# Kernel optimization log

Measured on AMD Instinct MI355X. Metric: run time of the kernel, lower is better.

Reference implementation:

```python
import jax, jax.numpy as jnp
import numpy as np


def setup_inputs() -> dict:
    key = jax.random.key(0)
    k1, k2, k3, k4 = jax.random.split(key, 4)
    B, S, I, O, G = 4, 2048, 4096, 11008, 128
    x = jax.random.normal(k1, (B, S, I), dtype=jnp.float32)
    # unpacked int4 codes in [0, 16)
    weight_q = jax.random.randint(k2, (O, I), 0, 16, dtype=jnp.int32)
    scales = jax.random.uniform(k3, (I // G, O, 1), minval=0.001, maxval=0.02)
    zeros = jax.random.normal(k4, (I // G, O, 1)) * 0.01
    scales_and_zeros = jnp.concatenate([scales, zeros], axis=-1).astype(jnp.bfloat16)
    return {"x": x, "weight_q": weight_q, "scales_and_zeros": scales_and_zeros, "groupsize": G}


def reference(x, weight_q, scales_and_zeros, groupsize):
    # Dequantize: w[o, g*gs + j] = (q - 8) * scale[g, o] + zero[g, o], in bf16
    O, I = weight_q.shape
    G = I // groupsize
    q = weight_q.reshape(O, G, groupsize).astype(jnp.bfloat16)  # [O, G, gs]
    s = scales_and_zeros[:, :, 0].T[:, :, None]  # [O, G, 1]
    z = scales_and_zeros[:, :, 1].T[:, :, None]  # [O, G, 1]
    w = ((q - 8.0) * s + z).reshape(O, I)  # bf16 dequantized weight
    xb = x.astype(jnp.bfloat16).reshape(-1, I)
    y = jnp.matmul(xb, w.T)  # [N, O] in bf16 (matches precision=bf16)
    y = y.astype(x.dtype)
    return y.reshape(x.shape[:-1] + (O,))
```

## Files before the change

### kernel.cpp

```cpp
#include <hip/hip_runtime.h>
#include <cstdint>
#include <cstddef>

#define N_ 8192
#define K_ 4096
#define O_ 11008
#define NT_ (K_ / 32)

typedef __bf16 bf16x8 __attribute__((ext_vector_type(8)));
typedef float f32x4 __attribute__((ext_vector_type(4)));

__device__ __forceinline__ uint16_t f2bf(float f) {
    uint32_t u = __float_as_uint(f);
    u += 0x7fffu + ((u >> 16) & 1u);
    return (uint16_t)(u >> 16);
}
__device__ __forceinline__ float bf2f(uint16_t b) {
    return __uint_as_float(((uint32_t)b) << 16);
}
__device__ __forceinline__ float bfr(float f) { return bf2f(f2bf(f)); }

__device__ __forceinline__ void async_cp16(const uint16_t* gsrc, uint16_t* ldst) {
    __builtin_amdgcn_global_load_lds(
        (__attribute__((address_space(1))) void*)gsrc,
        (__attribute__((address_space(3))) void*)ldst, 16, 0, 0);
}

__global__ __launch_bounds__(256) void xcast(const float* __restrict__ X,
                                             uint16_t* __restrict__ Xb) {
    const size_t n8 = (size_t)N_ * K_ / 8;
    size_t i = (size_t)blockIdx.x * 256u + threadIdx.x;
    const size_t stride = (size_t)gridDim.x * 256u;
    for (; i < n8; i += stride) {
        float4 a = ((const float4*)X)[2 * i];
        float4 b = ((const float4*)X)[2 * i + 1];
        union { uint16_t u[8]; uint4 v; } r;
        r.u[0] = f2bf(a.x); r.u[1] = f2bf(a.y); r.u[2] = f2bf(a.z); r.u[3] = f2bf(a.w);
        r.u[4] = f2bf(b.x); r.u[5] = f2bf(b.y); r.u[6] = f2bf(b.z); r.u[7] = f2bf(b.w);
        ((uint4*)Xb)[i] = r.v;
    }
}

__global__ __launch_bounds__(256) void wdeq(const int* __restrict__ Q,
                                            const float* __restrict__ SZ,
                                            uint16_t* __restrict__ Wb) {
    const size_t n8 = (size_t)O_ * K_ / 8;
    size_t i = (size_t)blockIdx.x * 256u + threadIdx.x;
    const size_t stride = (size_t)gridDim.x * 256u;
    for (; i < n8; i += stride) {
        const size_t e = i * 8;
        const size_t o = e >> 12;
        const uint32_t g = ((uint32_t)e >> 7) & 31;
        const float2 sz = ((const float2*)SZ)[(size_t)g * O_ + o];
        const float s = bfr(sz.x);
        const float z = bfr(sz.y);
        int4 qa = ((const int4*)Q)[2 * i];
        int4 qb = ((const int4*)Q)[2 * i + 1];
        int qs[8] = {qa.x, qa.y, qa.z, qa.w, qb.x, qb.y, qb.z, qb.w};
        union { uint16_t u[8]; uint4 v; } r;
#pragma unroll
        for (int j = 0; j < 8; ++j) {
            r.u[j] = f2bf(bfr((float)(qs[j] - 8) * s) + z);
        }
        ((uint4*)Wb)[i] = r.v;
    }
}

__global__ __launch_bounds__(512, 2) void gemm_mfma1b(const uint16_t* __restrict__ A,
                                                      const uint16_t* __restrict__ B,
                                                      float* __restrict__ C) {
    __shared__ uint16_t sA[4][256 * 32];
    __shared__ uint16_t sB[4][256 * 32];

    const int tid = threadIdx.x;
    const int l = tid & 63;
    const int w = tid >> 6;
    const int wm = w >> 2;
    const int wn = w & 3;
    const int n0 = blockIdx.x * 256;
    const int o0 = blockIdx.y * 256;

    const int gk = (((tid & 3) ^ ((tid >> 3) & 3)) & 3) * 8;
    const int sr0 = tid >> 2;
    const uint16_t* gA0 = A + (size_t)(n0 + sr0) * K_ + gk;
    const uint16_t* gA1 = A + (size_t)(n0 + 128 + sr0) * K_ + gk;
    const uint16_t* gB0 = B + (size_t)(o0 + sr0) * K_ + gk;
    const uint16_t* gB1 = B + (size_t)(o0 + 128 + sr0) * K_ + gk;
    const int ldst = tid * 8;

    const int lr = l & 15;
    const int cph = (((l >> 4) ^ ((l >> 1) & 3)) & 3) * 8;

    f32x4 acc[8][4] = {};

#define STAGE_A(j)                                                      \
    {                                                                   \
        const size_t ko = (size_t)(j) * 32;                             \
        uint16_t* d = &sA[(j) & 3][ldst];                               \
        async_cp16(gA0 + ko, d);                                        \
        async_cp16(gA1 + ko, d + 4096);                                 \
    }
#define STAGE_B(j)                                                      \
    {                                                                   \
        const size_t ko = (size_t)(j) * 32;                             \
        uint16_t* d = &sB[(j) & 3][ldst];                               \
        async_cp16(gB0 + ko, d);                                        \
        async_cp16(gB1 + ko, d + 4096);                                 \
    }

    STAGE_A(0) STAGE_B(0)
    STAGE_A(1) STAGE_B(1)
    STAGE_A(2) STAGE_B(2)

    for (int j = 0; j < NT_; ++j) {
        if (j < NT_ - 2)       asm volatile("s_waitcnt vmcnt(8)" ::: "memory");
        else if (j == NT_ - 2) asm volatile("s_waitcnt vmcnt(4)" ::: "memory");
        else                   asm volatile("s_waitcnt vmcnt(0)" ::: "memory");
        __builtin_amdgcn_s_barrier();

        const uint16_t* tA = sA[j & 3];
        const uint16_t* tB = sB[j & 3];

        bf16x8 bfrag[4], afrag[8];
#pragma unroll
        for (int n = 0; n < 4; ++n)
            bfrag[n] = *(const bf16x8*)&tB[(wn * 64 + n * 16 + lr) * 32 + cph];
#pragma unroll
        for (int m = 0; m < 8; ++m)
            afrag[m] = *(const bf16x8*)&tA[(wm * 128 + m * 16 + lr) * 32 + cph];
        if (j < NT_ - 3) {
            STAGE_A(j + 3)
            STAGE_B(j + 3)
        }
        __builtin_amdgcn_s_setprio(1);
#pragma unroll
        for (int m = 0; m < 8; ++m)
#pragma unroll
            for (int n = 0; n < 4; ++n)
                acc[m][n] = __builtin_amdgcn_mfma_f32_16x16x32_bf16(afrag[m], bfrag[n], acc[m][n], 0, 0, 0);
        __builtin_amdgcn_s_setprio(0);
    }
#undef STAGE_A
#undef STAGE_B

    const int rbase = (l >> 4) * 4;
#pragma unroll
    for (int m = 0; m < 8; ++m) {
#pragma unroll
        for (int n = 0; n < 4; ++n) {
#pragma unroll
            for (int r = 0; r < 4; ++r) {
                const size_t row = (size_t)(n0 + wm * 128 + m * 16 + rbase + r);
                C[row * O_ + (o0 + wn * 64 + n * 16 + lr)] = bfr(acc[m][n][r]);
            }
        }
    }
}

__global__ __launch_bounds__(256) void gemm_probe_f32sz(const float* __restrict__ X,
                                                        const int* __restrict__ Q,
                                                        const float* __restrict__ SZf,
                                                        float* __restrict__ C) {
    __shared__ float xs[32][64];
    __shared__ float ws[32][64];
    const int tid = threadIdx.x;
    const int n0 = blockIdx.x * 64;
    const int o0 = blockIdx.y * 64;
    const int tn = tid >> 4;
    const int to = tid & 15;
    const int srow = tid >> 2;
    const int skq = (tid & 3) * 8;

    float acc[4][4] = {};

    for (int k0 = 0; k0 < K_; k0 += 32) {
        {
            const float4* xp = (const float4*)(X + (size_t)(n0 + srow) * K_ + k0 + skq);
            float4 a = xp[0], b = xp[1];
            float v[8] = {a.x, a.y, a.z, a.w, b.x, b.y, b.z, b.w};
#pragma unroll
            for (int j = 0; j < 8; ++j) xs[skq + j][srow] = bfr(v[j]);
        }
        {
            const int o = o0 + srow;
            const uint32_t g = (uint32_t)k0 >> 7;
            const size_t p = (size_t)g * O_ + o;
            const float s = bfr(SZf[2 * p]);
            const float z = bfr(SZf[2 * p + 1]);
            const int4* qp = (const int4*)(Q + (size_t)o * K_ + k0 + skq);
            int4 qa = qp[0], qb = qp[1];
            int qs[8] = {qa.x, qa.y, qa.z, qa.w, qb.x, qb.y, qb.z, qb.w};
#pragma unroll
            for (int j = 0; j < 8; ++j) {
                float w1 = bfr((float)(qs[j] - 8) * s);
                ws[skq + j][srow] = bfr(w1 + z);
            }
        }
        __syncthreads();

#pragma unroll 8
        for (int kk = 0; kk < 32; ++kk) {
            const float4 xv = *(const float4*)&xs[kk][tn * 4];
            const float4 wv = *(const float4*)&ws[kk][to * 4];
            const float xa[4] = {xv.x, xv.y, xv.z, xv.w};
            const float wa[4] = {wv.x, wv.y, wv.z, wv.w};
#pragma unroll
            for (int i = 0; i < 4; ++i)
#pragma unroll
                for (int j = 0; j < 4; ++j)
                    acc[i][j] = fmaf(xa[i], wa[j], acc[i][j]);
        }
        __syncthreads();
    }

#pragma unroll
    for (int i = 0; i < 4; ++i) {
        const size_t row = (size_t)(n0 + tn * 4 + i);
#pragma unroll
        for (int j = 0; j < 4; ++j) {
            C[row * O_ + (o0 + to * 4 + j)] = bfr(acc[i][j]);
        }
    }
}

__global__ __launch_bounds__(256) void sentinel_fill(float* __restrict__ C, size_t n, float v) {
    size_t i = (size_t)blockIdx.x * 256u + threadIdx.x;
    size_t stride = (size_t)gridDim.x * 256u;
    for (; i < n; i += stride) C[i] = v;
}

extern "C" void kernel_launch(void* const* d_in, const int* in_sizes, int n_in,
                              void* d_out, int out_size, void* d_ws, size_t ws_size,
                              hipStream_t stream) {
    const float* x = (const float*)d_in[0];
    const int* q = (const int*)d_in[1];
    const float* szf = (const float*)d_in[2];
    float* out = (float*)d_out;

    float sentinel = 0.0f;
    if (n_in < 3)                         sentinel = 1000.0f;
    else if (in_sizes[0] != 33554432)     sentinel = 2000.0f;
    else if (in_sizes[1] != 45088768)     sentinel = 3000.0f;
    else if (in_sizes[2] != 704512)       sentinel = 4000.0f;
    else if (out_size   != 90177536)      sentinel = 5000.0f;

    if (sentinel != 0.0f) {
        sentinel_fill<<<8192, 256, 0, stream>>>(out, (size_t)out_size, sentinel);
        return;
    }

    const size_t xb_bytes = (size_t)N_ * K_ * 2;
    const size_t wb_bytes = (size_t)O_ * K_ * 2;

    if (ws_size >= xb_bytes + wb_bytes) {
        uint16_t* Xb = (uint16_t*)d_ws;
        uint16_t* Wb = (uint16_t*)((char*)d_ws + xb_bytes);
        xcast<<<4096, 256, 0, stream>>>(x, Xb);
        wdeq<<<4096, 256, 0, stream>>>(q, szf, Wb);
        dim3 grid(N_ / 256, O_ / 256);
        gemm_mfma1b<<<grid, 512, 0, stream>>>(Xb, Wb, out);
    } else {
        dim3 grid(N_ / 64, O_ / 64);
        gemm_probe_f32sz<<<grid, 256, 0, stream>>>(x, q, szf, out);
    }
}
```

Baseline: 1.244 ms.

## Software-pipeline LDS fragment reads ahead of MFMA in the GEMM main loop

Restructures the GEMM K-loop so the LDS fragments for the next tile are loaded right after the barrier. The MFMAs of the current iteration then run on fragments already held in registers, and the global-to-LDS staging for tile j+3 is issued before the MFMA block. The last iterations are peeled so the vmcnt waits stay correct. The aim is to hide LDS read latency and barrier stalls behind MFMA execution, at the cost of larger register live ranges and some possible WAR hazards on the fragment registers.

```diff
diff --git a/kernel.cpp b/kernel.cpp
--- a/kernel.cpp
+++ b/kernel.cpp
@@ -66,9 +66,9 @@
     }
 }
 
-__global__ __launch_bounds__(512, 2) void gemm_mfma1b(const uint16_t* __restrict__ A,
-                                                      const uint16_t* __restrict__ B,
-                                                      float* __restrict__ C) {
+__global__ __launch_bounds__(512, 2) void gemm_pipe(const uint16_t* __restrict__ A,
+                                                    const uint16_t* __restrict__ B,
+                                                    float* __restrict__ C) {
     __shared__ uint16_t sA[4][256 * 32];
     __shared__ uint16_t sB[4][256 * 32];
 
@@ -92,56 +92,63 @@
     const int cph = (((l >> 4) ^ ((l >> 1) & 3)) & 3) * 8;
 
     f32x4 acc[8][4] = {};
-
-#define STAGE_A(j)                                                      \
+    bf16x8 fa[8], fb[4];
+
+#define STAGE_AB(j)                                                     \
     {                                                                   \
         const size_t ko = (size_t)(j) * 32;                             \
-        uint16_t* d = &sA[(j) & 3][ldst];                               \
-        async_cp16(gA0 + ko, d);                                        \
-        async_cp16(gA1 + ko, d + 4096);                                 \
-    }
-#define STAGE_B(j)                                                      \
+        const int sl = (j) & 3;                                         \
+        uint16_t* dA = &sA[sl][ldst];                                   \
+        uint16_t* dB = &sB[sl][ldst];                                   \
+        async_cp16(gA0 + ko, dA);                                       \
+        async_cp16(gA1 + ko, dA + 4096);                                \
+        async_cp16(gB0 + ko, dB);                                       \
+        async_cp16(gB1 + ko, dB + 4096);                                \
+    }
+
+#define RD_FRAGS(slot)                                                  \
     {                                                                   \
-        const size_t ko = (size_t)(j) * 32;                             \
-        uint16_t* d = &sB[(j) & 3][ldst];                               \
-        async_cp16(gB0 + ko, d);                                        \
-        async_cp16(gB1 + ko, d + 4096);                                 \
-    }
-
-    STAGE_A(0) STAGE_B(0)
-    STAGE_A(1) STAGE_B(1)
-    STAGE_A(2) STAGE_B(2)
-
-    for (int j = 0; j < NT_; ++j) {
-        if (j < NT_ - 2)       asm volatile("s_waitcnt vmcnt(8)" ::: "memory");
-        else if (j == NT_ - 2) asm volatile("s_waitcnt vmcnt(4)" ::: "memory");
-        else                   asm volatile("s_waitcnt vmcnt(0)" ::: "memory");
+        const uint16_t* tB = sB[slot];                                  \
+        const uint16_t* tA = sA[slot];                                  \
+        _Pragma("unroll") for (int n = 0; n < 4; ++n)                   \
+            fb[n] = *(const bf16x8*)&tB[(wn * 64 + n * 16 + lr) * 32 + cph]; \
+        _Pragma("unroll") for (int m = 0; m < 8; ++m)                   \
+            fa[m] = *(const bf16x8*)&tA[(wm * 128 + m * 16 + lr) * 32 + cph]; \
+    }
+
+#define MFMA_ALL                                                        \
+    __builtin_amdgcn_s_setprio(1);                                      \
+    _Pragma("unroll") for (int m = 0; m < 8; ++m)                       \
+        _Pragma("unroll") for (int n = 0; n < 4; ++n)                   \
+            acc[m][n] = __builtin_amdgcn_mfma_f32_16x16x32_bf16(        \
+                fa[m], fb[n], acc[m][n], 0, 0, 0);                      \
+    __builtin_amdgcn_s_setprio(0);
+
+    STAGE_AB(0) STAGE_AB(1) STAGE_AB(2)
+    asm volatile("s_waitcnt vmcnt(8)" ::: "memory");
+    __builtin_amdgcn_s_barrier();
+    RD_FRAGS(0)
+
+    for (int j = 0; j < NT_ - 3; ++j) {
+        STAGE_AB(j + 3)
+        MFMA_ALL
+        asm volatile("s_waitcnt vmcnt(8)" ::: "memory");
         __builtin_amdgcn_s_barrier();
-
-        const uint16_t* tA = sA[j & 3];
-        const uint16_t* tB = sB[j & 3];
-
-        bf16x8 bfrag[4], afrag[8];
-#pragma unroll
-        for (int n = 0; n < 4; ++n)
-            bfrag[n] = *(const bf16x8*)&tB[(wn * 64 + n * 16 + lr) * 32 + cph];
-#pragma unroll
-        for (int m = 0; m < 8; ++m)
-            afrag[m] = *(const bf16x8*)&tA[(wm * 128 + m * 16 + lr) * 32 + cph];
-        if (j < NT_ - 3) {
-            STAGE_A(j + 3)
-            STAGE_B(j + 3)
-        }
-        __builtin_amdgcn_s_setprio(1);
-#pragma unroll
-        for (int m = 0; m < 8; ++m)
-#pragma unroll
-            for (int n = 0; n < 4; ++n)
-                acc[m][n] = __builtin_amdgcn_mfma_f32_16x16x32_bf16(afrag[m], bfrag[n], acc[m][n], 0, 0, 0);
-        __builtin_amdgcn_s_setprio(0);
-    }
-#undef STAGE_A
-#undef STAGE_B
+        RD_FRAGS((j + 1) & 3)
+    }
+    MFMA_ALL
+    asm volatile("s_waitcnt vmcnt(4)" ::: "memory");
+    __builtin_amdgcn_s_barrier();
+    RD_FRAGS((NT_ - 2) & 3)
+    MFMA_ALL
+    asm volatile("s_waitcnt vmcnt(0)" ::: "memory");
+    __builtin_amdgcn_s_barrier();
+    RD_FRAGS((NT_ - 1) & 3)
+    MFMA_ALL
+
+#undef STAGE_AB
+#undef RD_FRAGS
+#undef MFMA_ALL
 
     const int rbase = (l >> 4) * 4;
 #pragma unroll
@@ -258,7 +265,7 @@
         xcast<<<4096, 256, 0, stream>>>(x, Xb);
         wdeq<<<4096, 256, 0, stream>>>(q, szf, Wb);
         dim3 grid(N_ / 256, O_ / 256);
-        gemm_mfma1b<<<grid, 512, 0, stream>>>(Xb, Wb, out);
+        gemm_pipe<<<grid, 512, 0, stream>>>(Xb, Wb, out);
     } else {
         dim3 grid(N_ / 64, O_ / 64);
         gemm_probe_f32sz<<<grid, 256, 0, stream>>>(x, q, szf, out);
```

New measurement: 1.225 ms. Within noise of the previous version (-1.6%).
